# Optimization experiments

Measured on AMD Instinct MI355X. Metric: run time of the kernel, lower is better.

Reference implementation:

```python
import jax, jax.numpy as jnp
import numpy as np

D_MODEL = 1024
N_HEADS = 16
D_HEAD = D_MODEL // N_HEADS
N_LAYERS = 12
VOCAB = 32000
TAU = 30.0
B, L = 8, 512
NEG = -1e9


def _layernorm(x, gamma, beta):
    m = x.mean(-1, keepdims=True)
    v = ((x - m) ** 2).mean(-1, keepdims=True)
    return (x - m) / jnp.sqrt(v + 1e-5) * gamma + beta


def _pos_embed(length, d):
    # sinusoidal positional embedding, matching the torch _get_pos_embed
    position = jnp.arange(length, dtype=jnp.float32)[:, None]
    div_term = jnp.exp(jnp.arange(0, d, 2, dtype=jnp.float32) * (-jnp.log(jnp.float32(10000.0)) / d))
    pe = jnp.zeros((length, d), dtype=jnp.float32)
    pe = pe.at[:, 0::2].set(jnp.sin(position * div_term))
    pe = pe.at[:, 1::2].set(jnp.cos(position * div_term))
    return pe


def setup_inputs() -> dict:
    key = jax.random.key(0)
    ks = jax.random.split(key, 18)
    HD = N_HEADS * D_HEAD
    inp = {}
    inp["input_ids"] = jax.random.randint(ks[0], (B, L), 0, VOCAB)
    inp["attention_mask"] = jnp.ones((B, L), dtype=jnp.int32)
    s_d = 1.0 / np.sqrt(D_MODEL)
    inp["W_vocab"] = jax.random.normal(ks[1], (D_MODEL, VOCAB), jnp.float32) * s_d
    inp["W_devocab"] = jax.random.normal(ks[2], (D_MODEL, VOCAB), jnp.float32) * s_d
    inp["WQ"] = jax.random.normal(ks[3], (N_LAYERS, HD, D_MODEL), jnp.float32) * s_d
    inp["WK"] = jax.random.normal(ks[4], (N_LAYERS, HD, D_MODEL), jnp.float32) * s_d
    inp["WV"] = jax.random.normal(ks[5], (N_LAYERS, HD, D_MODEL), jnp.float32) * s_d
    inp["W_O"] = jax.random.normal(ks[6], (N_LAYERS, D_MODEL, HD), jnp.float32) / np.sqrt(HD)
    inp["gamma1"] = jnp.ones((N_LAYERS, D_MODEL), jnp.float32)
    inp["beta1"] = jnp.zeros((N_LAYERS, D_MODEL), jnp.float32)
    inp["gamma2"] = jnp.ones((N_LAYERS, D_MODEL), jnp.float32)
    inp["beta2"] = jnp.zeros((N_LAYERS, D_MODEL), jnp.float32)
    inp["W_up"] = jax.random.normal(ks[7], (N_LAYERS, D_MODEL, 4 * D_MODEL), jnp.float32) * s_d
    inp["b_up"] = jnp.zeros((N_LAYERS, 4 * D_MODEL), jnp.float32)
    inp["W_down"] = jax.random.normal(ks[8], (N_LAYERS, 4 * D_MODEL, D_MODEL), jnp.float32) / np.sqrt(4 * D_MODEL)
    inp["b_down"] = jnp.zeros((N_LAYERS, D_MODEL), jnp.float32)
    inp["gamma_f"] = jnp.ones((D_MODEL,), jnp.float32)
    inp["beta_f"] = jnp.zeros((D_MODEL,), jnp.float32)
    return inp


def reference(input_ids, attention_mask, W_vocab, W_devocab, WQ, WK, WV, W_O,
              gamma1, beta1, gamma2, beta2, W_up, b_up, W_down, b_down,
              gamma_f, beta_f):
    b, l = input_ids.shape
    # F.embedding(ids, W_vocab.t()) -> rows of W_vocab.T
    x = jnp.take(W_vocab.T, input_ids, axis=0) + _pos_embed(l, D_MODEL)[None]
    causal = jnp.triu(jnp.ones((l, l), dtype=bool), 1)          # [L,L]
    pad = (attention_mask == 0)[:, None, None, :]                # [B,1,1,L]
    mask = causal[None, None] | pad                              # [B,1,L,L] broadcast over heads
    scale = 1.0 / np.sqrt(D_HEAD)
    for i in range(N_LAYERS):
        u = _layernorm(x, gamma1[i], beta1[i])
        q = (u @ WQ[i].T).reshape(b, l, N_HEADS, D_HEAD)
        k = (u @ WK[i].T).reshape(b, l, N_HEADS, D_HEAD)
        v = (u @ WV[i].T).reshape(b, l, N_HEADS, D_HEAD)
        S = jnp.einsum('blhd,bmhd->bhlm', q, k) * scale
        S = TAU * jnp.tanh(S)                                    # tanh-clipped mode
        S = jnp.where(mask, NEG, S)
        A = jax.nn.softmax(S, axis=-1)
        attn = jnp.einsum('bhlm,bmhd->blhd', A, v).reshape(b, l, N_HEADS * D_HEAD)
        z1 = x + attn @ W_O[i].T
        v1 = _layernorm(z1, gamma2[i], beta2[i])
        h = jax.nn.gelu(v1 @ W_up[i] + b_up[i], approximate=False)
        x = z1 + h @ W_down[i] + b_down[i]
    x_final = _layernorm(x, gamma_f, beta_f)
    return x_final @ W_devocab
```

## Files before the change

### kernel.cpp

```cpp
#include <hip/hip_runtime.h>
#include <math.h>

#define D_MODEL 1024
#define NHEADS 16
#define DHEAD 64
#define NLAYERS 12
#define VOCAB 32000
#define BATCH 8
#define SEQ 512
#define NTOK (BATCH*SEQ)

using short8 = __attribute__((ext_vector_type(8))) short;
using fx4    = __attribute__((ext_vector_type(4))) float;

#define GLL16(g, l) __builtin_amdgcn_global_load_lds( \
    (const __attribute__((address_space(1))) unsigned int*)(g), \
    (__attribute__((address_space(3))) unsigned int*)(l), 16, 0, 0)

__device__ __forceinline__ unsigned short f2bf(float f) {
  union { float f; unsigned u; } v; v.f = f;
  unsigned r = v.u + 0x7FFFu + ((v.u >> 16) & 1u);
  return (unsigned short)(r >> 16);
}
__device__ __forceinline__ float bf2f(unsigned short u) {
  union { unsigned u; float f; } v; v.u = ((unsigned)u) << 16;
  return v.f;
}
__device__ __forceinline__ void split2(float x, unsigned short& h, unsigned short& l) {
  h = f2bf(x);
  l = f2bf(x - bf2f(h));
}
__device__ __forceinline__ float gelu_exact(float x) {
  return 0.5f * x * (1.f + erff(x * 0.70710678118654752f));
}


__global__ __launch_bounds__(256) void cvt_qkv_split(const float* __restrict__ WQ,
    const float* __restrict__ WK, const float* __restrict__ WV,
    unsigned short* __restrict__ out)
{
  const long total = 12L * 3072 * 256;
  const long stride = (long)gridDim.x * blockDim.x;
  for (long t = (long)blockIdx.x * blockDim.x + threadIdx.x; t < total; t += stride) {
    const long layer = t / (3072L * 256);
    const long rem = t - layer * (3072L * 256);
    const int n = (int)(rem >> 8);
    const int k4 = (int)(rem & 255);
    const float* src;
    if (n < 1024)       src = WQ + ((size_t)layer * 1024 + n) * 1024;
    else if (n < 2048)  src = WK + ((size_t)layer * 1024 + (n - 1024)) * 1024;
    else                src = WV + ((size_t)layer * 1024 + (n - 2048)) * 1024;
    const float4 v = *(const float4*)(src + k4 * 4);
    ushort4 h, l; unsigned short a, b;
    split2(v.x, a, b); h.x = a; l.x = b;
    split2(v.y, a, b); h.y = a; l.y = b;
    split2(v.z, a, b); h.z = a; l.z = b;
    split2(v.w, a, b); h.w = a; l.w = b;
    unsigned short* dst = out + ((size_t)layer * 3072 + n) * 2048 + k4 * 4;
    *(ushort4*)dst = h;
    *(ushort4*)(dst + 1024) = l;
  }
}

__global__ __launch_bounds__(256) void cvt_split(const float* __restrict__ in,
    unsigned short* __restrict__ out, long rows, int K)
{
  const int K4 = K >> 2;
  const long total = rows * K4;
  const long stride = (long)gridDim.x * blockDim.x;
  for (long t = (long)blockIdx.x * blockDim.x + threadIdx.x; t < total; t += stride) {
    const long r = t / K4;
    const int k4 = (int)(t - r * K4);
    const float4 v = *(const float4*)(in + r * K + k4 * 4);
    ushort4 h, l; unsigned short a, b;
    split2(v.x, a, b); h.x = a; l.x = b;
    split2(v.y, a, b); h.y = a; l.y = b;
    split2(v.z, a, b); h.z = a; l.z = b;
    split2(v.w, a, b); h.w = a; l.w = b;
    unsigned short* dst = out + r * 2 * K + k4 * 4;
    *(ushort4*)dst = h;
    *(ushort4*)(dst + K) = l;
  }
}

__global__ __launch_bounds__(256) void transpose_cvt_split(const float* __restrict__ in,
    unsigned short* __restrict__ out, int R, int C)
{
  __shared__ float tile[32][33];
  in  += (size_t)blockIdx.z * R * C;
  out += (size_t)blockIdx.z * 2 * R * C;
  const int r0 = blockIdx.y * 32, c0 = blockIdx.x * 32;
  const int tr = threadIdx.x >> 5, tc = threadIdx.x & 31;
#pragma unroll
  for (int i = 0; i < 4; ++i)
    tile[tr + i * 8][tc] = in[(size_t)(r0 + tr + i * 8) * C + c0 + tc];
  __syncthreads();
#pragma unroll
  for (int i = 0; i < 4; ++i) {
    unsigned short h, l;
    split2(tile[tc][tr + i * 8], h, l);
    const size_t o = (size_t)(c0 + tr + i * 8) * 2 * R + r0 + tc;
    out[o] = h;
    out[o + R] = l;
  }
}

__global__ __launch_bounds__(256) void transpose_cvt(const float* __restrict__ in,
    unsigned short* __restrict__ out, int R, int C)
{
  __shared__ float tile[32][33];
  const int r0 = blockIdx.y * 32, c0 = blockIdx.x * 32;
  const int tr = threadIdx.x >> 5, tc = threadIdx.x & 31;
#pragma unroll
  for (int i = 0; i < 4; ++i)
    tile[tr + i * 8][tc] = in[(size_t)(r0 + tr + i * 8) * C + c0 + tc];
  __syncthreads();
#pragma unroll
  for (int i = 0; i < 4; ++i)
    out[(size_t)(c0 + tr + i * 8) * R + r0 + tc] = f2bf(tile[tc][tr + i * 8]);
}


__global__ __launch_bounds__(256) void embed_kernel(const int* __restrict__ ids,
    const float* __restrict__ Wv, float* __restrict__ x)
{
  const int t = blockIdx.x;
  const int id = ids[t];
  const int l = t & (SEQ - 1);
  const float pos = (float)l;
  const int d0 = threadIdx.x * 4;
  const float i0 = (float)(d0 >> 1);
  const float f0 = expf(-0.017988946039016f * i0);
  const float f1 = expf(-0.017988946039016f * (i0 + 1.f));
  const float a0 = pos * f0, a1 = pos * f1;
  float4 v;
  v.x = Wv[(size_t)(d0 + 0) * VOCAB + id] + sinf(a0);
  v.y = Wv[(size_t)(d0 + 1) * VOCAB + id] + cosf(a0);
  v.z = Wv[(size_t)(d0 + 2) * VOCAB + id] + sinf(a1);
  v.w = Wv[(size_t)(d0 + 3) * VOCAB + id] + cosf(a1);
  ((float4*)(x + (size_t)t * 1024))[threadIdx.x] = v;
}


__global__ __launch_bounds__(256) void layernorm_split(const float* __restrict__ x,
    const float* __restrict__ g, const float* __restrict__ be,
    unsigned short* __restrict__ out)
{
  const int row = blockIdx.x;
  const float4 v = ((const float4*)(x + (size_t)row * 1024))[threadIdx.x];
  float s = v.x + v.y + v.z + v.w;
  float q = v.x * v.x + v.y * v.y + v.z * v.z + v.w * v.w;
#pragma unroll
  for (int o = 32; o; o >>= 1) { s += __shfl_xor(s, o); q += __shfl_xor(q, o); }
  __shared__ float ss[4], qq[4];
  const int w = threadIdx.x >> 6;
  if ((threadIdx.x & 63) == 0) { ss[w] = s; qq[w] = q; }
  __syncthreads();
  s = ss[0] + ss[1] + ss[2] + ss[3];
  q = qq[0] + qq[1] + qq[2] + qq[3];
  const float mean = s * (1.f / 1024.f);
  const float var = q * (1.f / 1024.f) - mean * mean;
  const float rstd = rsqrtf(var + 1e-5f);
  const float4 gv = ((const float4*)g)[threadIdx.x];
  const float4 bv = ((const float4*)be)[threadIdx.x];
  float4 y;
  y.x = (v.x - mean) * rstd * gv.x + bv.x;
  y.y = (v.y - mean) * rstd * gv.y + bv.y;
  y.z = (v.z - mean) * rstd * gv.z + bv.z;
  y.w = (v.w - mean) * rstd * gv.w + bv.w;
  ushort4 h4, l4; unsigned short a, b;
  split2(y.x, a, b); h4.x = a; l4.x = b;
  split2(y.y, a, b); h4.y = a; l4.y = b;
  split2(y.z, a, b); h4.z = a; l4.z = b;
  split2(y.w, a, b); h4.w = a; l4.w = b;
  unsigned short* dst = out + (size_t)row * 2048 + threadIdx.x * 4;
  *(ushort4*)dst = h4;
  *(ushort4*)(dst + 1024) = l4;
}


template<int EPI, int SPLIT, int SWAPG>
__global__ __launch_bounds__(256) void gemm_bt(
    const unsigned short* __restrict__ A, const unsigned short* __restrict__ B,
    float* __restrict__ Cf, unsigned short* __restrict__ Cb,
    const float* __restrict__ bias, const float* __restrict__ res,
    int M, int N, int K)
{
  __shared__ __align__(16) unsigned short As[128 * 64];
  __shared__ __align__(16) unsigned short Bs[128 * 64];
  const int tid = threadIdx.x;
  const int lane = tid & 63, w = tid >> 6;
  const int wr = w >> 1, wc = w & 1;
  const int bxi = SWAPG ? blockIdx.y : blockIdx.x;
  const int byi = SWAPG ? blockIdx.x : blockIdx.y;
  const int brow = byi * 128, bcol = bxi * 128;

  const int SA = 2 * K;
  const int SB = (SPLIT == 3) ? 2 * K : K;
  const int KEFF = SPLIT * K;
  fx4 acc[4][4];
  const fx4 zero = {0.f, 0.f, 0.f, 0.f};
#pragma unroll
  for (int i = 0; i < 4; ++i)
#pragma unroll
    for (int j = 0; j < 4; ++j) acc[i][j] = zero;

  const unsigned short* Ab = A + (size_t)brow * SA;
  const unsigned short* Bb = B + (size_t)bcol * SB;

  for (int k0 = 0; k0 < KEFF; k0 += 64) {
    int ka, kb;
    if (SPLIT == 3) {
      ka = (k0 < 2 * K) ? k0 : k0 - 2 * K;
      kb = (k0 < K) ? k0 : k0 - K;
    } else {
      ka = k0;
      kb = (k0 < K) ? k0 : k0 - K;
    }
    const unsigned short* Aseg = Ab + ka;
    const unsigned short* Bseg = Bb + kb;
#pragma unroll
    for (int it = 0; it < 4; ++it) {
      const int idx = it * 256 + tid;
      const int r = idx >> 3;
      const int c = ((idx & 7) ^ (r & 7)) * 8;
      GLL16(&Aseg[(size_t)r * SA + c], &As[idx * 8]);
      GLL16(&Bseg[(size_t)r * SB + c], &Bs[idx * 8]);
    }
    __syncthreads();
#pragma unroll
    for (int kk = 0; kk < 2; ++kk) {
      short8 af[4], bfv[4];
      const int slot = ((kk * 4 + (lane >> 4)) ^ (lane & 7)) * 8;
#pragma unroll
      for (int f = 0; f < 4; ++f)
        af[f] = *(const short8*)&As[(wr * 64 + f * 16 + (lane & 15)) * 64 + slot];
#pragma unroll
      for (int f = 0; f < 4; ++f)
        bfv[f] = *(const short8*)&Bs[(wc * 64 + f * 16 + (lane & 15)) * 64 + slot];
#pragma unroll
      for (int i = 0; i < 4; ++i)
#pragma unroll
        for (int j = 0; j < 4; ++j)
          acc[i][j] = __builtin_amdgcn_mfma_f32_16x16x32_bf16(af[i], bfv[j], acc[i][j], 0, 0, 0);
    }
    __syncthreads();
  }

  const int r0 = brow + wr * 64 + (lane >> 4) * 4;
  const int c0 = bcol + wc * 64 + (lane & 15);
#pragma unroll
  for (int i = 0; i < 4; ++i) {
#pragma unroll
    for (int j = 0; j < 4; ++j) {
      const int cc = c0 + j * 16;
#pragma unroll
      for (int qi = 0; qi < 4; ++qi) {
        const int rr = r0 + i * 16 + qi;
        const size_t off = (size_t)rr * N + cc;
        const float val = acc[i][j][qi];
        if (EPI == 0) {
          Cf[off] = val;
        } else if (EPI == 2) {
          Cf[off] = res[off] + val;
        } else if (EPI == 3) {
          unsigned short hh, ll;
          split2(gelu_exact(val + bias[cc]), hh, ll);
          Cb[(size_t)rr * (2 * N) + cc] = hh;
          Cb[(size_t)rr * (2 * N) + N + cc] = ll;
        } else {
          Cf[off] = res[off] + val + bias[cc];
        }
      }
    }
  }
}


__global__ __launch_bounds__(256, 4) void attn_kernel(
    const float* __restrict__ qkvf,
    const int* __restrict__ amask,
    unsigned short* __restrict__ out2)
{
  const int bid = blockIdx.x;
  const int qt = 7 - (bid & 7);
  const int h  = (bid >> 3) & 15;
  const int b  = bid >> 7;

  __shared__ __align__(16) unsigned short Kh[64 * 64];
  __shared__ __align__(16) unsigned short Kl[64 * 64];
  __shared__ __align__(16) unsigned short Vt[64 * 64];
  __shared__ __align__(16) unsigned short Ph[4][16 * 64];
  __shared__ __align__(16) unsigned short Pl[4][16 * 64];

  const int tid = threadIdx.x, lane = tid & 63, w = tid >> 6;
  const size_t base = (size_t)b * SEQ;
  const int qrow0 = qt * 64 + w * 16;

  short8 qh[2], ql[2];
  {
    const int row = qrow0 + (lane & 15);
    const float* qp = &qkvf[(base + row) * 3072 + h * 64 + (lane >> 4) * 8];
#pragma unroll
    for (int ks = 0; ks < 2; ++ks) {
      const float4 a = *(const float4*)(qp + ks * 32);
      const float4 c = *(const float4*)(qp + ks * 32 + 4);
      short8 hh, ll; unsigned short th, tl;
      split2(a.x, th, tl); hh[0] = (short)th; ll[0] = (short)tl;
      split2(a.y, th, tl); hh[1] = (short)th; ll[1] = (short)tl;
      split2(a.z, th, tl); hh[2] = (short)th; ll[2] = (short)tl;
      split2(a.w, th, tl); hh[3] = (short)th; ll[3] = (short)tl;
      split2(c.x, th, tl); hh[4] = (short)th; ll[4] = (short)tl;
      split2(c.y, th, tl); hh[5] = (short)th; ll[5] = (short)tl;
      split2(c.z, th, tl); hh[6] = (short)th; ll[6] = (short)tl;
      split2(c.w, th, tl); hh[7] = (short)th; ll[7] = (short)tl;
      qh[ks] = hh; ql[ks] = ll;
    }
  }

  fx4 oacc[4];
  float sumr[4] = {0.f, 0.f, 0.f, 0.f};
#pragma unroll
  for (int j = 0; j < 4; ++j) oacc[j] = (fx4){0.f, 0.f, 0.f, 0.f};

  for (int kc = 0; kc <= qt; ++kc) {
    const int c0 = kc * 64;
    __syncthreads();
#pragma unroll
    for (int it = 0; it < 4; ++it) {
      const int idx = it * 256 + tid;
      const int key = idx >> 4, c4 = idx & 15;
      const float4 kv = *(const float4*)&qkvf[(base + c0 + key) * 3072 + 1024 + h * 64 + c4 * 4];
      ushort4 kh4, kl4;
      split2(kv.x, kh4.x, kl4.x); split2(kv.y, kh4.y, kl4.y);
      split2(kv.z, kh4.z, kl4.z); split2(kv.w, kh4.w, kl4.w);
      const int sl = (((c4 >> 1) ^ (key & 7)) * 8 + (c4 & 1) * 4);
      *(ushort4*)&Kh[key * 64 + sl] = kh4;
      *(ushort4*)&Kl[key * 64 + sl] = kl4;
      const float4 vv = *(const float4*)&qkvf[(base + c0 + key) * 3072 + 2048 + h * 64 + c4 * 4];
      {
        const int d0 = c4 * 4;
        Vt[(d0 + 0) * 64 + ((key >> 3) ^ ((d0 + 0) & 7)) * 8 + (key & 7)] = f2bf(vv.x);
        Vt[(d0 + 1) * 64 + ((key >> 3) ^ ((d0 + 1) & 7)) * 8 + (key & 7)] = f2bf(vv.y);
        Vt[(d0 + 2) * 64 + ((key >> 3) ^ ((d0 + 2) & 7)) * 8 + (key & 7)] = f2bf(vv.z);
        Vt[(d0 + 3) * 64 + ((key >> 3) ^ ((d0 + 3) & 7)) * 8 + (key & 7)] = f2bf(vv.w);
      }
    }
    __syncthreads();

    const bool diag = (kc == qt);
#pragma unroll
    for (int j = 0; j < 4; ++j) {
      fx4 sacc = {0.f, 0.f, 0.f, 0.f};
#pragma unroll
      for (int ks = 0; ks < 2; ++ks) {
        const int krow = j * 16 + (lane & 15);
        const int soff = ((ks * 4 + (lane >> 4)) ^ (krow & 7)) * 8;
        const short8 bh = *(const short8*)&Kh[krow * 64 + soff];
        const short8 bl = *(const short8*)&Kl[krow * 64 + soff];
        sacc = __builtin_amdgcn_mfma_f32_16x16x32_bf16(qh[ks], bh, sacc, 0, 0, 0);
        sacc = __builtin_amdgcn_mfma_f32_16x16x32_bf16(ql[ks], bh, sacc, 0, 0, 0);
        sacc = __builtin_amdgcn_mfma_f32_16x16x32_bf16(qh[ks], bl, sacc, 0, 0, 0);
      }
      const int key = c0 + j * 16 + (lane & 15);
      const int am = amask[b * SEQ + key];
      const int col = j * 16 + (lane & 15);
#pragma unroll
      for (int qi = 0; qi < 4; ++qi) {
        const int prow = (lane >> 4) * 4 + qi;
        const int row = qrow0 + prow;
        const float e = __expf(sacc[qi] * 0.25f);
        const float S = 30.f - 60.f / (e + 1.f);
        float p = __expf(S);
        const bool valid = (!diag || (key <= row)) && (am != 0);
        p = valid ? p : 0.f;
        sumr[qi] += p;
        unsigned short ph_, pl_;
        split2(p, ph_, pl_);
        const int ss = (((col >> 3) ^ (prow & 7)) * 8) + (col & 7);
        Ph[w][prow * 64 + ss] = ph_;
        Pl[w][prow * 64 + ss] = pl_;
      }
    }

#pragma unroll
    for (int jd = 0; jd < 4; ++jd) {
#pragma unroll
      for (int ks = 0; ks < 2; ++ks) {
        const int drow = jd * 16 + (lane & 15);
        const int soff = ((ks * 4 + (lane >> 4)) ^ (drow & 7)) * 8;
        const short8 bv = *(const short8*)&Vt[drow * 64 + soff];
        const int psoff = ((ks * 4 + (lane >> 4)) ^ (lane & 7)) * 8;
        const short8 pa = *(const short8*)&Ph[w][(lane & 15) * 64 + psoff];
        const short8 pb = *(const short8*)&Pl[w][(lane & 15) * 64 + psoff];
        oacc[jd] = __builtin_amdgcn_mfma_f32_16x16x32_bf16(pa, bv, oacc[jd], 0, 0, 0);
        oacc[jd] = __builtin_amdgcn_mfma_f32_16x16x32_bf16(pb, bv, oacc[jd], 0, 0, 0);
      }
    }
  }

#pragma unroll
  for (int qi = 0; qi < 4; ++qi) {
    float cs = sumr[qi];
#pragma unroll
    for (int o = 1; o <= 8; o <<= 1) cs += __shfl_xor(cs, o);
    sumr[qi] = cs;
  }
#pragma unroll
  for (int jd = 0; jd < 4; ++jd) {
#pragma unroll
    for (int qi = 0; qi < 4; ++qi) {
      const int row = qrow0 + (lane >> 4) * 4 + qi;
      const int d = jd * 16 + (lane & 15);
      const float o = oacc[jd][qi] / sumr[qi];
      unsigned short hh, ll;
      split2(o, hh, ll);
      out2[(base + row) * 2048 + h * 64 + d] = hh;
      out2[(base + row) * 2048 + 1024 + h * 64 + d] = ll;
    }
  }
}

extern "C" void kernel_launch(void* const* d_in, const int* in_sizes, int n_in,
                              void* d_out, int out_size, void* d_ws, size_t ws_size,
                              hipStream_t stream) {
  const int*   ids       = (const int*)d_in[0];
  const int*   amask     = (const int*)d_in[1];
  const float* W_vocab   = (const float*)d_in[2];
  const float* W_devocab = (const float*)d_in[3];
  const float* WQ        = (const float*)d_in[4];
  const float* WK        = (const float*)d_in[5];
  const float* WV        = (const float*)d_in[6];
  const float* W_O       = (const float*)d_in[7];
  const float* gamma1    = (const float*)d_in[8];
  const float* beta1     = (const float*)d_in[9];
  const float* gamma2    = (const float*)d_in[10];
  const float* beta2     = (const float*)d_in[11];
  const float* W_up      = (const float*)d_in[12];
  const float* b_up      = (const float*)d_in[13];
  const float* W_down    = (const float*)d_in[14];
  const float* b_down    = (const float*)d_in[15];
  const float* gamma_f   = (const float*)d_in[16];
  const float* beta_f    = (const float*)d_in[17];

  char* p = (char*)d_ws;
  auto alloc = [&](size_t bytes) { char* r = p; p += (bytes + 255) & ~(size_t)255; return r; };

  unsigned short* WQKV2 = (unsigned short*)alloc((size_t)NLAYERS * 3072 * 2048 * 2);
  unsigned short* WO2   = (unsigned short*)alloc((size_t)NLAYERS * 1024 * 2048 * 2);
  unsigned short* WUp2  = (unsigned short*)alloc((size_t)NLAYERS * 4096 * 2048 * 2);
  unsigned short* WDn2  = (unsigned short*)alloc((size_t)NLAYERS * 1024 * 8192 * 2);
  unsigned short* WDev1 = (unsigned short*)alloc((size_t)VOCAB * 1024 * 2);
  float* x    = (float*)alloc((size_t)NTOK * 1024 * 4);
  float* z1   = (float*)alloc((size_t)NTOK * 1024 * 4);
  unsigned short* u2    = (unsigned short*)alloc((size_t)NTOK * 2048 * 2);
  float* qkvf = (float*)alloc((size_t)NTOK * 3072 * 4);
  unsigned short* attn2 = (unsigned short*)alloc((size_t)NTOK * 2048 * 2);
  unsigned short* h2    = (unsigned short*)alloc((size_t)NTOK * 8192 * 2);
  (void)ws_size; (void)in_sizes; (void)n_in; (void)out_size;

  cvt_qkv_split<<<2048, 256, 0, stream>>>(WQ, WK, WV, WQKV2);
  cvt_split<<<2048, 256, 0, stream>>>(W_O, WO2, (long)NLAYERS * 1024, 1024);
  transpose_cvt_split<<<dim3(4096 / 32, 1024 / 32, NLAYERS), 256, 0, stream>>>(W_up, WUp2, 1024, 4096);
  transpose_cvt_split<<<dim3(1024 / 32, 4096 / 32, NLAYERS), 256, 0, stream>>>(W_down, WDn2, 4096, 1024);
  transpose_cvt<<<dim3(VOCAB / 32, 1024 / 32, 1), 256, 0, stream>>>(W_devocab, WDev1, 1024, VOCAB);

  embed_kernel<<<NTOK, 256, 0, stream>>>(ids, W_vocab, x);

  for (int l = 0; l < NLAYERS; ++l) {
    layernorm_split<<<NTOK, 256, 0, stream>>>(x, gamma1 + l * 1024, beta1 + l * 1024, u2);
    gemm_bt<0, 3, 0><<<dim3(3072 / 128, NTOK / 128), 256, 0, stream>>>(
        u2, WQKV2 + (size_t)l * 3072 * 2048, qkvf, nullptr, nullptr, nullptr,
        NTOK, 3072, 1024);
    attn_kernel<<<BATCH * NHEADS * 8, 256, 0, stream>>>(qkvf, amask, attn2);
    gemm_bt<2, 3, 0><<<dim3(1024 / 128, NTOK / 128), 256, 0, stream>>>(
        attn2, WO2 + (size_t)l * 1024 * 2048, z1, nullptr, nullptr, x,
        NTOK, 1024, 1024);
    layernorm_split<<<NTOK, 256, 0, stream>>>(z1, gamma2 + l * 1024, beta2 + l * 1024, u2);
    gemm_bt<3, 3, 0><<<dim3(4096 / 128, NTOK / 128), 256, 0, stream>>>(
        u2, WUp2 + (size_t)l * 4096 * 2048, nullptr, h2, b_up + l * 4096, nullptr,
        NTOK, 4096, 1024);
    gemm_bt<4, 3, 0><<<dim3(1024 / 128, NTOK / 128), 256, 0, stream>>>(
        h2, WDn2 + (size_t)l * 1024 * 8192, x, nullptr, b_down + l * 1024, z1,
        NTOK, 1024, 4096);
  }

  layernorm_split<<<NTOK, 256, 0, stream>>>(x, gamma_f, beta_f, u2);
  gemm_bt<0, 2, 1><<<dim3(NTOK / 128, VOCAB / 128), 256, 0, stream>>>(
      u2, WDev1, (float*)d_out, nullptr, nullptr, nullptr,
      NTOK, VOCAB, 1024);
}
```

Measured before the change: 9.360 ms.

## Use 32x32x16 MFMA tiles in GEMM and add low-part V correction in attention

Switches the GEMM inner loop from 16x16x32 bf16 MFMAs to 32x32x16 MFMAs. This halves the number of fragment LDS reads per MFMA and remaps the epilogue to the 32x32 output layout. Attention now splits V into high and low bf16 parts and adds a third MFMA using the low part, which improves accuracy. That adds LDS, MFMA work and shared memory, and attention occupancy is lowered to 3 blocks per SM.

```diff
diff --git a/kernel.cpp b/kernel.cpp
--- a/kernel.cpp
+++ b/kernel.cpp
@@ -12,6 +12,7 @@
 
 using short8 = __attribute__((ext_vector_type(8))) short;
 using fx4    = __attribute__((ext_vector_type(4))) float;
+using fx16   = __attribute__((ext_vector_type(16))) float;
 
 #define GLL16(g, l) __builtin_amdgcn_global_load_lds( \
     (const __attribute__((address_space(1))) unsigned int*)(g), \
@@ -198,12 +199,13 @@
   const int SA = 2 * K;
   const int SB = (SPLIT == 3) ? 2 * K : K;
   const int KEFF = SPLIT * K;
-  fx4 acc[4][4];
-  const fx4 zero = {0.f, 0.f, 0.f, 0.f};
-#pragma unroll
-  for (int i = 0; i < 4; ++i)
-#pragma unroll
-    for (int j = 0; j < 4; ++j) acc[i][j] = zero;
+  fx16 acc[2][2];
+#pragma unroll
+  for (int i = 0; i < 2; ++i)
+#pragma unroll
+    for (int j = 0; j < 2; ++j)
+#pragma unroll
+      for (int e = 0; e < 16; ++e) acc[i][j][e] = 0.f;
 
   const unsigned short* Ab = A + (size_t)brow * SA;
   const unsigned short* Bb = B + (size_t)bcol * SB;
@@ -229,36 +231,36 @@
     }
     __syncthreads();
 #pragma unroll
-    for (int kk = 0; kk < 2; ++kk) {
-      short8 af[4], bfv[4];
-      const int slot = ((kk * 4 + (lane >> 4)) ^ (lane & 7)) * 8;
-#pragma unroll
-      for (int f = 0; f < 4; ++f)
-        af[f] = *(const short8*)&As[(wr * 64 + f * 16 + (lane & 15)) * 64 + slot];
-#pragma unroll
-      for (int f = 0; f < 4; ++f)
-        bfv[f] = *(const short8*)&Bs[(wc * 64 + f * 16 + (lane & 15)) * 64 + slot];
-#pragma unroll
-      for (int i = 0; i < 4; ++i)
-#pragma unroll
-        for (int j = 0; j < 4; ++j)
-          acc[i][j] = __builtin_amdgcn_mfma_f32_16x16x32_bf16(af[i], bfv[j], acc[i][j], 0, 0, 0);
+    for (int ks = 0; ks < 4; ++ks) {
+      const int slot = ((ks * 2 + (lane >> 5)) ^ (lane & 7)) * 8;
+      short8 af[2], bfv[2];
+#pragma unroll
+      for (int ti = 0; ti < 2; ++ti)
+        af[ti] = *(const short8*)&As[(wr * 64 + ti * 32 + (lane & 31)) * 64 + slot];
+#pragma unroll
+      for (int tj = 0; tj < 2; ++tj)
+        bfv[tj] = *(const short8*)&Bs[(wc * 64 + tj * 32 + (lane & 31)) * 64 + slot];
+#pragma unroll
+      for (int ti = 0; ti < 2; ++ti)
+#pragma unroll
+        for (int tj = 0; tj < 2; ++tj)
+          acc[ti][tj] = __builtin_amdgcn_mfma_f32_32x32x16_bf16(af[ti], bfv[tj], acc[ti][tj], 0, 0, 0);
     }
     __syncthreads();
   }
 
-  const int r0 = brow + wr * 64 + (lane >> 4) * 4;
-  const int c0 = bcol + wc * 64 + (lane & 15);
-#pragma unroll
-  for (int i = 0; i < 4; ++i) {
-#pragma unroll
-    for (int j = 0; j < 4; ++j) {
-      const int cc = c0 + j * 16;
-#pragma unroll
-      for (int qi = 0; qi < 4; ++qi) {
-        const int rr = r0 + i * 16 + qi;
+  const int cl = lane & 31;
+  const int rb = 4 * (lane >> 5);
+#pragma unroll
+  for (int ti = 0; ti < 2; ++ti) {
+#pragma unroll
+    for (int tj = 0; tj < 2; ++tj) {
+      const int cc = bcol + wc * 64 + tj * 32 + cl;
+#pragma unroll
+      for (int reg = 0; reg < 16; ++reg) {
+        const int rr = brow + wr * 64 + ti * 32 + (reg & 3) + 8 * (reg >> 2) + rb;
         const size_t off = (size_t)rr * N + cc;
-        const float val = acc[i][j][qi];
+        const float val = acc[ti][tj][reg];
         if (EPI == 0) {
           Cf[off] = val;
         } else if (EPI == 2) {
@@ -277,7 +279,7 @@
 }
 
 
-__global__ __launch_bounds__(256, 4) void attn_kernel(
+__global__ __launch_bounds__(256, 3) void attn_kernel(
     const float* __restrict__ qkvf,
     const int* __restrict__ amask,
     unsigned short* __restrict__ out2)
@@ -290,6 +292,7 @@
   __shared__ __align__(16) unsigned short Kh[64 * 64];
   __shared__ __align__(16) unsigned short Kl[64 * 64];
   __shared__ __align__(16) unsigned short Vt[64 * 64];
+  __shared__ __align__(16) unsigned short Vl[64 * 64];
   __shared__ __align__(16) unsigned short Ph[4][16 * 64];
   __shared__ __align__(16) unsigned short Pl[4][16 * 64];
 
@@ -340,10 +343,15 @@
       const float4 vv = *(const float4*)&qkvf[(base + c0 + key) * 3072 + 2048 + h * 64 + c4 * 4];
       {
         const int d0 = c4 * 4;
-        Vt[(d0 + 0) * 64 + ((key >> 3) ^ ((d0 + 0) & 7)) * 8 + (key & 7)] = f2bf(vv.x);
-        Vt[(d0 + 1) * 64 + ((key >> 3) ^ ((d0 + 1) & 7)) * 8 + (key & 7)] = f2bf(vv.y);
-        Vt[(d0 + 2) * 64 + ((key >> 3) ^ ((d0 + 2) & 7)) * 8 + (key & 7)] = f2bf(vv.z);
-        Vt[(d0 + 3) * 64 + ((key >> 3) ^ ((d0 + 3) & 7)) * 8 + (key & 7)] = f2bf(vv.w);
+        unsigned short vh_, vl_;
+        split2(vv.x, vh_, vl_);
+        { const int o = (d0 + 0) * 64 + ((key >> 3) ^ ((d0 + 0) & 7)) * 8 + (key & 7); Vt[o] = vh_; Vl[o] = vl_; }
+        split2(vv.y, vh_, vl_);
+        { const int o = (d0 + 1) * 64 + ((key >> 3) ^ ((d0 + 1) & 7)) * 8 + (key & 7); Vt[o] = vh_; Vl[o] = vl_; }
+        split2(vv.z, vh_, vl_);
+        { const int o = (d0 + 2) * 64 + ((key >> 3) ^ ((d0 + 2) & 7)) * 8 + (key & 7); Vt[o] = vh_; Vl[o] = vl_; }
+        split2(vv.w, vh_, vl_);
+        { const int o = (d0 + 3) * 64 + ((key >> 3) ^ ((d0 + 3) & 7)) * 8 + (key & 7); Vt[o] = vh_; Vl[o] = vl_; }
       }
     }
     __syncthreads();
@@ -389,12 +397,14 @@
       for (int ks = 0; ks < 2; ++ks) {
         const int drow = jd * 16 + (lane & 15);
         const int soff = ((ks * 4 + (lane >> 4)) ^ (drow & 7)) * 8;
-        const short8 bv = *(const short8*)&Vt[drow * 64 + soff];
+        const short8 bv  = *(const short8*)&Vt[drow * 64 + soff];
+        const short8 bvl = *(const short8*)&Vl[drow * 64 + soff];
         const int psoff = ((ks * 4 + (lane >> 4)) ^ (lane & 7)) * 8;
         const short8 pa = *(const short8*)&Ph[w][(lane & 15) * 64 + psoff];
         const short8 pb = *(const short8*)&Pl[w][(lane & 15) * 64 + psoff];
         oacc[jd] = __builtin_amdgcn_mfma_f32_16x16x32_bf16(pa, bv, oacc[jd], 0, 0, 0);
         oacc[jd] = __builtin_amdgcn_mfma_f32_16x16x32_bf16(pb, bv, oacc[jd], 0, 0, 0);
+        oacc[jd] = __builtin_amdgcn_mfma_f32_16x16x32_bf16(pa, bvl, oacc[jd], 0, 0, 0);
       }
     }
   }
```

New measurement: 8.806 ms. -5.9%, faster.
